# Kernel tuning notes

Measured on AMD Instinct MI355X. Metric: run time of the kernel, lower is better.

Reference implementation:

```python
import jax, jax.numpy as jnp
import numpy as np

B, T, C, H = 8, 2048, 1024, 128  # batch, seq (== block_size), embed dim, head size


def setup_inputs() -> dict:
    key = jax.random.key(0)
    kx, kq, kk, kv = jax.random.split(key, 4)
    x = jax.random.normal(kx, (B, T, C), dtype=jnp.float32)
    # torch Linear(no bias) weights: [head_size, in_features], applied as x @ W.T
    s = 1.0 / np.sqrt(C)
    Wq = jax.random.normal(kq, (H, C), dtype=jnp.float32) * s
    Wk = jax.random.normal(kk, (H, C), dtype=jnp.float32) * s
    Wv = jax.random.normal(kv, (H, C), dtype=jnp.float32) * s
    return {"x": x, "Wq": Wq, "Wk": Wk, "Wv": Wv}


def reference(x, Wq, Wk, Wv):
    # projections: [B,T,C] @ [C,H] -> [B,T,H]
    q = jnp.einsum('btc,hc->bth', x, Wq)
    k = jnp.einsum('btc,hc->bth', x, Wk)
    v = jnp.einsum('btc,hc->bth', x, Wv)
    scale = k.shape[-1] ** -0.5
    # scores [B,T,T], causal mask, softmax in fp32 (autocast disabled in original)
    scores = jnp.einsum('bqh,bkh->bqk', q, k) * scale
    causal = jnp.tril(jnp.ones((T, T), dtype=bool))
    scores = jnp.where(causal, scores, -jnp.inf)
    attn = jax.nn.softmax(scores.astype(jnp.float32), axis=-1)
    # dropout_rate = 0.0 -> identity
    out = jnp.einsum('bqk,bkh->bqh', attn.astype(v.dtype), v)
    return out
```

## Files before the change

kernel.cpp:

```cpp
#include <hip/hip_runtime.h>
#include <hip/hip_bf16.h>

constexpr int NB = 8;
constexpr int T  = 2048;
constexpr int C  = 1024;
constexpr int Hd = 128;

typedef short bf16x8 __attribute__((ext_vector_type(8)));
typedef float floatx4 __attribute__((ext_vector_type(4)));

__device__ __forceinline__ ushort f2bf(float x) {
    return __builtin_bit_cast(ushort, __float2bfloat16(x));
}
__device__ __forceinline__ float bf2f(ushort u) {
    unsigned int x = ((unsigned int)u) << 16;
    return __builtin_bit_cast(float, x);
}
__device__ __forceinline__ void async16(ushort* lds, const ushort* g) {
    __builtin_amdgcn_global_load_lds(
        (const __attribute__((address_space(1))) unsigned int*)g,
        (__attribute__((address_space(3))) unsigned int*)lds, 16, 0, 0);
}

__global__ __launch_bounds__(256) void convert_xw(
    const float* __restrict__ X, const float* __restrict__ Wq,
    const float* __restrict__ Wk, const float* __restrict__ Wv,
    ushort* __restrict__ Xb, ushort* __restrict__ Wb)
{
    int bid = blockIdx.x;
    if (bid < 8192) {
        size_t i = ((size_t)bid * 256 + threadIdx.x) * 8;
        float4 a = *(const float4*)&X[i];
        float4 b = *(const float4*)&X[i + 4];
        bf16x8 o;
        o[0] = (short)f2bf(a.x); o[1] = (short)f2bf(a.y);
        o[2] = (short)f2bf(a.z); o[3] = (short)f2bf(a.w);
        o[4] = (short)f2bf(b.x); o[5] = (short)f2bf(b.y);
        o[6] = (short)f2bf(b.z); o[7] = (short)f2bf(b.w);
        *(bf16x8*)&Xb[i] = o;
    } else {
        int g = (bid - 8192) * 256 + threadIdx.x;
        size_t base = (size_t)g * 8;
        int sel = (int)(base >> 17);
        const float* W = sel == 0 ? Wq : (sel == 1 ? Wk : Wv);
        float s = (sel == 0) ? 0.12751744f : 1.0f;
        size_t off = base - (size_t)sel * 131072;
        float4 a = *(const float4*)&W[off];
        float4 b = *(const float4*)&W[off + 4];
        bf16x8 o;
        o[0] = (short)f2bf(a.x * s); o[1] = (short)f2bf(a.y * s);
        o[2] = (short)f2bf(a.z * s); o[3] = (short)f2bf(a.w * s);
        o[4] = (short)f2bf(b.x * s); o[5] = (short)f2bf(b.y * s);
        o[6] = (short)f2bf(b.z * s); o[7] = (short)f2bf(b.w * s);
        *(bf16x8*)&Wb[base] = o;
    }
}

__global__ __launch_bounds__(256) void qkv_gemm(
    const ushort* __restrict__ Xb, const ushort* __restrict__ Wb,
    ushort* __restrict__ Qo, ushort* __restrict__ Ko, ushort* __restrict__ Vt)
{
    __shared__ ushort SM[24576];
    ushort* Al = SM;
    ushort* Bl = SM + 16384;
    const int m0 = blockIdx.x * 128;
    const int n0 = blockIdx.y * 64;
    const int tid = threadIdx.x, lane = tid & 63, wave = tid >> 6;
    const int quad = lane >> 4, colL = lane & 15;
    const int wm = (wave & 1) * 64, wn = (wave >> 1) * 32;
    const int lr4 = lane >> 4;
    const int cg  = lane & 15;

    floatx4 acc[4][2] = {};

    for (int k0 = 0; k0 < C; k0 += 128) {
        for (int t = 0; t < 8; ++t) {
            int q = wave * 8 + t;
            int row = q * 4 + lr4;
            async16(&Al[q * 512 + lane * 8],
                    &Xb[(size_t)(m0 + row) * C + k0 + ((cg ^ (row & 7)) * 8)]);
        }
        for (int t = 0; t < 4; ++t) {
            int q = wave * 4 + t;
            int row = q * 4 + lr4;
            async16(&Bl[q * 512 + lane * 8],
                    &Wb[(size_t)(n0 + row) * C + k0 + ((cg ^ (row & 7)) * 8)]);
        }
        __syncthreads();

        for (int kk = 0; kk < 4; ++kk) {
            bf16x8 af[4], bfr[2];
            for (int mt = 0; mt < 4; ++mt)
                af[mt] = *(const bf16x8*)
                    &Al[(wm + mt * 16 + colL) * 128 + (((kk * 4 + quad) ^ (colL & 7))) * 8];
            for (int nt = 0; nt < 2; ++nt)
                bfr[nt] = *(const bf16x8*)
                    &Bl[(wn + nt * 16 + colL) * 128 + (((kk * 4 + quad) ^ (colL & 7))) * 8];
            for (int mt = 0; mt < 4; ++mt)
                for (int nt = 0; nt < 2; ++nt)
                    acc[mt][nt] = __builtin_amdgcn_mfma_f32_16x16x32_bf16(
                        af[mt], bfr[nt], acc[mt][nt], 0, 0, 0);
        }
        __syncthreads();
    }

    const int sel = n0 >> 7;
    const int h0 = n0 & 127;
    if (sel < 2) {
        ushort* dst = sel == 0 ? Qo : Ko;
        for (int mt = 0; mt < 4; ++mt)
            for (int nt = 0; nt < 2; ++nt)
                for (int r = 0; r < 4; ++r) {
                    int row = m0 + wm + mt * 16 + quad * 4 + r;
                    int h = h0 + wn + nt * 16 + colL;
                    dst[(size_t)row * Hd + h] = f2bf(acc[mt][nt][r]);
                }
    } else {
        ushort* TL = SM;
        for (int mt = 0; mt < 4; ++mt)
            for (int nt = 0; nt < 2; ++nt)
                for (int r = 0; r < 4; ++r)
                    TL[(wm + mt * 16 + quad * 4 + r) * 66 + wn + nt * 16 + colL] =
                        f2bf(acc[mt][nt][r]);
        __syncthreads();
        const int b = m0 >> 11, tb = m0 & 2047;
        const int h = tid & 63, tq = tid >> 6;
        for (int st = 0; st < 4; ++st) {
            int t0 = tq * 32 + st * 8;
            bf16x8 o;
            for (int jx = 0; jx < 8; ++jx)
                o[jx] = (short)TL[(t0 + jx) * 66 + h];
            *(bf16x8*)&Vt[((size_t)b * Hd + h0 + h) * T + tb + t0] = o;
        }
    }
}

__global__ __launch_bounds__(256, 2) void attn_flash(
    const ushort* __restrict__ Q, const ushort* __restrict__ Kg,
    const ushort* __restrict__ Vt, float* __restrict__ out)
{
    __shared__ ushort Kl[128 * 128];
    __shared__ ushort Vl[128 * 128];

    const int tid = threadIdx.x, lane = tid & 63, wave = tid >> 6;
    const int quad = lane >> 4, colL = lane & 15;

    const int id = blockIdx.x;
    const int b = id & 7;
    const int qt = 31 - (id >> 3);
    const int q0 = qt * 64;
    const int cmax = (q0 + 63) >> 7;

    bf16x8 qa[4];
    {
        const ushort* qp =
            &Q[((size_t)b * T + q0 + wave * 16 + colL) * Hd + quad * 8];
        for (int ks = 0; ks < 4; ++ks)
            qa[ks] = *(const bf16x8*)&qp[ks * 32];
    }

    floatx4 Oacc[8] = {};
    float m_r[4], l_r[4];
    for (int rr = 0; rr < 4; ++rr) { m_r[rr] = -__builtin_inff(); l_r[rr] = 0.f; }

    const int r16 = tid >> 4, p16 = tid & 15;

    for (int c = 0; c <= cmax; ++c) {
        if (c > 0) __syncthreads();
        const int k0 = c * 128;
        for (int t = 0; t < 8; ++t) {
            int row = t * 16 + r16;
            async16(&Kl[t * 2048 + tid * 8],
                    &Kg[((size_t)b * T + k0 + row) * Hd + ((p16 ^ (row & 15)) * 8)]);
        }
        for (int t = 0; t < 8; ++t) {
            int hrow = t * 16 + r16;
            async16(&Vl[t * 2048 + tid * 8],
                    &Vt[((size_t)b * Hd + hrow) * T + k0 + ((p16 ^ (hrow & 15)) * 8)]);
        }
        __syncthreads();

        floatx4 accS[8] = {};
        for (int ks = 0; ks < 4; ++ks)
            for (int nt = 0; nt < 8; ++nt) {
                int krow = nt * 16 + colL;
                bf16x8 kb = *(const bf16x8*)&Kl[krow * 128 + (((ks * 4 + quad) ^ colL) * 8)];
                accS[nt] = __builtin_amdgcn_mfma_f32_16x16x32_bf16(qa[ks], kb, accS[nt], 0, 0, 0);
            }

        if (c == cmax) {
            for (int nt = 0; nt < 8; ++nt)
                for (int rr = 0; rr < 4; ++rr) {
                    int lrow = q0 + wave * 16 + quad * 4 + rr;
                    int lcol = k0 + nt * 16 + colL;
                    if (lcol > lrow) accS[nt][rr] = -__builtin_inff();
                }
        }
        __syncthreads();

        float sc[4];
        for (int rr = 0; rr < 4; ++rr) {
            float mx = accS[0][rr];
            for (int nt = 1; nt < 8; ++nt) mx = fmaxf(mx, accS[nt][rr]);
            for (int off = 1; off < 16; off <<= 1)
                mx = fmaxf(mx, __shfl_xor(mx, off, 64));
            float nm = fmaxf(m_r[rr], mx);
            sc[rr] = __builtin_amdgcn_exp2f(m_r[rr] - nm);
            m_r[rr] = nm;
        }
        for (int th = 0; th < 8; ++th)
            for (int rr = 0; rr < 4; ++rr)
                Oacc[th][rr] *= sc[rr];

        ushort* Pw = &Kl[wave * 2048];
        {
            float ls[4] = {0.f, 0.f, 0.f, 0.f};
            for (int nt = 0; nt < 8; ++nt)
                for (int rr = 0; rr < 4; ++rr) {
                    float p = __builtin_amdgcn_exp2f(accS[nt][rr] - m_r[rr]);
                    ls[rr] += p;
                    int prow = quad * 4 + rr;
                    Pw[prow * 128 + ((nt * 16 + colL) ^ ((prow & 7) << 4))] = f2bf(p);
                }
            for (int rr = 0; rr < 4; ++rr) {
                float s = ls[rr];
                for (int off = 1; off < 16; off <<= 1)
                    s += __shfl_xor(s, off, 64);
                l_r[rr] = l_r[rr] * sc[rr] + s;
            }
        }

        bf16x8 pa[4];
        {
            const int prow = colL;
            const int sw = (prow & 7) << 4;
            for (int ks = 0; ks < 4; ++ks)
                pa[ks] = *(const bf16x8*)&Pw[prow * 128 + ((ks * 32 + quad * 8) ^ sw)];
        }

        for (int ks = 0; ks < 4; ++ks)
            for (int th = 0; th < 8; ++th) {
                int hrow = th * 16 + colL;
                bf16x8 vb = *(const bf16x8*)&Vl[hrow * 128 + (((ks * 4 + quad) ^ colL) * 8)];
                Oacc[th] = __builtin_amdgcn_mfma_f32_16x16x32_bf16(pa[ks], vb, Oacc[th], 0, 0, 0);
            }
    }

    float inv[4];
    for (int rr = 0; rr < 4; ++rr) inv[rr] = 1.0f / l_r[rr];
    for (int th = 0; th < 8; ++th)
        for (int rr = 0; rr < 4; ++rr) {
            int row = q0 + wave * 16 + quad * 4 + rr;
            out[((size_t)b * T + row) * Hd + th * 16 + colL] = Oacc[th][rr] * inv[rr];
        }
}

extern "C" void kernel_launch(void* const* d_in, const int* in_sizes, int n_in,
                              void* d_out, int out_size, void* d_ws, size_t ws_size,
                              hipStream_t stream) {
    const float* x  = (const float*)d_in[0];
    const float* Wq = (const float*)d_in[1];
    const float* Wk = (const float*)d_in[2];
    const float* Wv = (const float*)d_in[3];
    float* out = (float*)d_out;

    char* w = (char*)d_ws;
    ushort* Xb = (ushort*)w;  w += (size_t)33554432;
    ushort* Wb = (ushort*)w;  w += (size_t)786432;
    ushort* Qb  = (ushort*)w;  w += (size_t)NB * T * Hd * 2;
    ushort* Kb  = (ushort*)w;  w += (size_t)NB * T * Hd * 2;
    ushort* Vtb = (ushort*)w;  w += (size_t)NB * T * Hd * 2;

    convert_xw<<<8384, 256, 0, stream>>>(x, Wq, Wk, Wv, Xb, Wb);
    qkv_gemm<<<dim3(128, 6), 256, 0, stream>>>(Xb, Wb, Qb, Kb, Vtb);
    attn_flash<<<256, 256, 0, stream>>>(Qb, Kb, Vtb, out);
}
```

Before: 166.0 us.

## Double-buffer K/V tiles in LDS and prefetch next chunk during compute

K and V LDS tiles become double-buffered. The next chunk's async global-to-LDS loads are issued right after the loop-top barrier, so they overlap the QK^T, softmax and PV work on the current chunk. The P tile moves from reusing the K buffer into its own per-wave buffer, which removes one __syncthreads per iteration. LDS use per block rises to about 144KB, so the requested two blocks per CU can no longer fit. With a grid of 256 blocks that may not matter on a large GPU.

```diff
diff --git a/kernel.cpp b/kernel.cpp
--- a/kernel.cpp
+++ b/kernel.cpp
@@ -139,8 +139,9 @@
     const ushort* __restrict__ Q, const ushort* __restrict__ Kg,
     const ushort* __restrict__ Vt, float* __restrict__ out)
 {
-    __shared__ ushort Kl[128 * 128];
-    __shared__ ushort Vl[128 * 128];
+    __shared__ ushort Kl[2][128 * 128];
+    __shared__ ushort Vl[2][128 * 128];
+    __shared__ ushort Pl[4][16 * 128];
 
     const int tid = threadIdx.x, lane = tid & 63, wave = tid >> 6;
     const int quad = lane >> 4, colL = lane & 15;
@@ -151,6 +152,20 @@
     const int q0 = qt * 64;
     const int cmax = (q0 + 63) >> 7;
 
+    const int r16 = tid >> 4, p16 = tid & 15;
+
+    {
+        for (int t = 0; t < 8; ++t) {
+            int row = t * 16 + r16;
+            async16(&Kl[0][t * 2048 + tid * 8],
+                    &Kg[((size_t)b * T + row) * Hd + ((p16 ^ (row & 15)) * 8)]);
+        }
+        for (int t = 0; t < 8; ++t) {
+            int hrow = t * 16 + r16;
+            async16(&Vl[0][t * 2048 + tid * 8],
+                    &Vt[((size_t)b * Hd + hrow) * T + ((p16 ^ (hrow & 15)) * 8)]);
+        }
+    }
     bf16x8 qa[4];
     {
         const ushort* qp =
@@ -163,32 +178,38 @@
     float m_r[4], l_r[4];
     for (int rr = 0; rr < 4; ++rr) { m_r[rr] = -__builtin_inff(); l_r[rr] = 0.f; }
 
-    const int r16 = tid >> 4, p16 = tid & 15;
+    ushort* Pw = &Pl[wave][0];
 
     for (int c = 0; c <= cmax; ++c) {
-        if (c > 0) __syncthreads();
-        const int k0 = c * 128;
-        for (int t = 0; t < 8; ++t) {
-            int row = t * 16 + r16;
-            async16(&Kl[t * 2048 + tid * 8],
-                    &Kg[((size_t)b * T + k0 + row) * Hd + ((p16 ^ (row & 15)) * 8)]);
-        }
-        for (int t = 0; t < 8; ++t) {
-            int hrow = t * 16 + r16;
-            async16(&Vl[t * 2048 + tid * 8],
-                    &Vt[((size_t)b * Hd + hrow) * T + k0 + ((p16 ^ (hrow & 15)) * 8)]);
-        }
-        __syncthreads();
+        const int cur = c & 1;
+        __syncthreads();
+
+        if (c < cmax) {
+            const int k0 = (c + 1) * 128;
+            const int nxt = cur ^ 1;
+            for (int t = 0; t < 8; ++t) {
+                int row = t * 16 + r16;
+                async16(&Kl[nxt][t * 2048 + tid * 8],
+                        &Kg[((size_t)b * T + k0 + row) * Hd + ((p16 ^ (row & 15)) * 8)]);
+            }
+            for (int t = 0; t < 8; ++t) {
+                int hrow = t * 16 + r16;
+                async16(&Vl[nxt][t * 2048 + tid * 8],
+                        &Vt[((size_t)b * Hd + hrow) * T + k0 + ((p16 ^ (hrow & 15)) * 8)]);
+            }
+        }
 
         floatx4 accS[8] = {};
         for (int ks = 0; ks < 4; ++ks)
             for (int nt = 0; nt < 8; ++nt) {
                 int krow = nt * 16 + colL;
-                bf16x8 kb = *(const bf16x8*)&Kl[krow * 128 + (((ks * 4 + quad) ^ colL) * 8)];
+                bf16x8 kb = *(const bf16x8*)
+                    &Kl[cur][krow * 128 + (((ks * 4 + quad) ^ colL) * 8)];
                 accS[nt] = __builtin_amdgcn_mfma_f32_16x16x32_bf16(qa[ks], kb, accS[nt], 0, 0, 0);
             }
 
         if (c == cmax) {
+            const int k0 = c * 128;
             for (int nt = 0; nt < 8; ++nt)
                 for (int rr = 0; rr < 4; ++rr) {
                     int lrow = q0 + wave * 16 + quad * 4 + rr;
@@ -196,7 +217,6 @@
                     if (lcol > lrow) accS[nt][rr] = -__builtin_inff();
                 }
         }
-        __syncthreads();
 
         float sc[4];
         for (int rr = 0; rr < 4; ++rr) {
@@ -212,7 +232,6 @@
             for (int rr = 0; rr < 4; ++rr)
                 Oacc[th][rr] *= sc[rr];
 
-        ushort* Pw = &Kl[wave * 2048];
         {
             float ls[4] = {0.f, 0.f, 0.f, 0.f};
             for (int nt = 0; nt < 8; ++nt)
@@ -241,7 +260,8 @@
         for (int ks = 0; ks < 4; ++ks)
             for (int th = 0; th < 8; ++th) {
                 int hrow = th * 16 + colL;
-                bf16x8 vb = *(const bf16x8*)&Vl[hrow * 128 + (((ks * 4 + quad) ^ colL) * 8)];
+                bf16x8 vb = *(const bf16x8*)
+                    &Vl[cur][hrow * 128 + (((ks * 4 + quad) ^ colL) * 8)];
                 Oacc[th] = __builtin_amdgcn_mfma_f32_16x16x32_bf16(pa[ks], vb, Oacc[th], 0, 0, 0);
             }
     }
```

After: 171.4 us. +3.2%, slower.
